# Kernel tuning notes

Hardware: AMD Instinct MI355X
Metric: run time of the kernel (lower is better)

The kernel has to match this reference:

```python
import jax, jax.numpy as jnp
import numpy as np

N = 50000   # num nodes
E = 400000  # num edges (avg degree 8)
D = 256     # in_channels
H = 256     # hidden_channels
C = 64      # out_channels
K = 2       # k_hops


def setup_inputs() -> dict:
    key = jax.random.key(0)
    ks = jax.random.split(key, 10)
    x = jax.random.normal(ks[0], (N, D), dtype=jnp.float32)
    edge_index = jax.random.randint(ks[1], (2, E), 0, N, dtype=jnp.int32)
    s = 0.05
    # per-hop linears of the single H2GCNConv (weights stored [in, out])
    W0 = jax.random.normal(ks[2], (D, H), jnp.float32) * s
    W1 = jax.random.normal(ks[3], (D, H), jnp.float32) * s
    W2 = jax.random.normal(ks[4], (D, H), jnp.float32) * s
    b0 = jnp.zeros((H,), jnp.float32)
    b1 = jnp.zeros((H,), jnp.float32)
    b2 = jnp.zeros((H,), jnp.float32)
    # classifier: h2_out_dim = H*(K+1) = 768 -> C
    Wc = jax.random.normal(ks[5], (H * (K + 1), C), jnp.float32) * s
    bc = jnp.zeros((C,), jnp.float32)
    return {"x": x, "edge_index": edge_index, "num_nodes": N,
            "W0": W0, "b0": b0, "W1": W1, "b1": b1, "W2": W2, "b2": b2,
            "Wc": Wc, "bc": bc}


def _normalize_adj(edge_index, num_nodes):
    # add self loops, then D^{-1/2} A D^{-1/2} edge weights
    loops = jnp.arange(num_nodes, dtype=edge_index.dtype)
    ei = jnp.concatenate([edge_index, jnp.stack([loops, loops])], axis=1)
    row, col = ei[0], ei[1]
    deg = jax.ops.segment_sum(jnp.ones(row.shape[0], jnp.float32), row,
                              num_segments=num_nodes)
    dis = jnp.where(deg > 0, deg ** -0.5, 0.0)  # inf -> 0 for isolated nodes
    return ei, dis[row] * dis[col]


def _sparse_mm(edge_index, edge_weight, x, num_nodes):
    # gather -> scale -> scatter-add (COO SpMM)
    row, col = edge_index[0], edge_index[1]
    msg = x[col] * edge_weight[:, None]  # [E', F]
    return jax.ops.segment_sum(msg, row, num_segments=num_nodes)


def reference(x, edge_index, num_nodes, W0, b0, W1, b1, W2, b2, Wc, bc):
    ei, ew = _normalize_adj(edge_index, num_nodes)
    # H2GCNConv: ego + k-hop aggregates, each through its own linear, concat
    outs = [x @ W0 + b0]
    cur = x
    for Wk, bk in ((W1, b1), (W2, b2)):
        cur = _sparse_mm(ei, ew, cur, num_nodes)
        outs.append(cur @ Wk + bk)
    h = jax.nn.relu(jnp.concatenate(outs, axis=1))  # [N, 3H]
    # dropout p=0 / eval mode -> identity
    return h @ Wc + bc
```

## Files before the change

kernel.cpp:

```cpp
#include <hip/hip_runtime.h>


#define FD 256
#define CO 64
#define SB 512

using frag_ab = __attribute__((ext_vector_type(8))) short;
using f32x4   = __attribute__((ext_vector_type(4))) float;
typedef unsigned short u16;
typedef unsigned int   u32;

__device__ __forceinline__ u16 f2bf(float f) {
    u32 u = __builtin_bit_cast(u32, f);
    return (u16)((u + 0x7FFFu + ((u >> 16) & 1u)) >> 16);
}
__device__ __forceinline__ float bfl(u32 packed) {
    return __builtin_bit_cast(float, packed << 16);
}
__device__ __forceinline__ float bfh(u32 packed) {
    return __builtin_bit_cast(float, packed & 0xFFFF0000u);
}

__device__ __forceinline__ void gll16(const void* g, void* l) {
    __builtin_amdgcn_global_load_lds(
        (const __attribute__((address_space(1))) u32*)g,
        (__attribute__((address_space(3))) u32*)l, 16, 0, 0);
}

#define BAR()  __builtin_amdgcn_s_barrier()
#define WLG0() asm volatile("s_waitcnt lgkmcnt(0)" ::: "memory")
#define WVM0() asm volatile("s_waitcnt vmcnt(0)" ::: "memory")
#define WVM2() asm volatile("s_waitcnt vmcnt(2)" ::: "memory")

__global__ void zerok(int4* __restrict__ deg4, int4* __restrict__ fill4, int n4) {
    int i = blockIdx.x * blockDim.x + threadIdx.x;
    int4 z = make_int4(0, 0, 0, 0);
    if (i < n4) { deg4[i] = z; fill4[i] = z; }
}
__global__ void count_kernel(const int* __restrict__ ei0, int* deg, int e) {
    int i = blockIdx.x * blockDim.x + threadIdx.x;
    if (i < e) atomicAdd(&deg[ei0[i]], 1);
}
__global__ void scan1(const int* __restrict__ deg, int* __restrict__ rowptr,
                      int* __restrict__ bsum, float* __restrict__ dis, int n) {
    __shared__ int sh[SB];
    int tid = threadIdx.x;
    int i = blockIdx.x * SB + tid;
    int v = (i < n) ? deg[i] + 1 : 0;
    if (i < n) dis[i] = rsqrtf((float)v);
    sh[tid] = v;
    __syncthreads();
    for (int off = 1; off < SB; off <<= 1) {
        int add = (tid >= off) ? sh[tid - off] : 0;
        __syncthreads();
        sh[tid] += add;
        __syncthreads();
    }
    if (i < n) rowptr[i] = sh[tid] - v;
    if (tid == SB - 1) bsum[blockIdx.x] = sh[tid];
}
__global__ void scan2(const int* __restrict__ bsum, int* __restrict__ bscan, int nb) {
    __shared__ int sh[128];
    int tid = threadIdx.x;
    int v = (tid < nb) ? bsum[tid] : 0;
    sh[tid] = v;
    __syncthreads();
    for (int off = 1; off < 128; off <<= 1) {
        int add = (tid >= off) ? sh[tid - off] : 0;
        __syncthreads();
        sh[tid] += add;
        __syncthreads();
    }
    if (tid < nb) bscan[tid] = sh[tid] - v;
    if (tid == nb - 1) bscan[nb] = sh[tid];
}
__global__ void scan3(int* rowptr, const int* __restrict__ bscan, int n, int nb) {
    int i = blockIdx.x * 256 + threadIdx.x;
    if (i < n) rowptr[i] += bscan[i / SB];
    if (i == n) rowptr[n] = bscan[nb];
}
__global__ void fill_kernel(const int* __restrict__ ei, const float* __restrict__ dis,
                            const int* __restrict__ rowptr, int* fill,
                            int2* __restrict__ cw, int e, int n) {
    int i = blockIdx.x * blockDim.x + threadIdx.x;
    if (i >= e + n) return;
    int r, c;
    if (i < e) { r = ei[i]; c = ei[e + i]; }
    else       { r = i - e; c = r; }
    float w = dis[r] * dis[c];
    int pos = rowptr[r] + atomicAdd(&fill[r], 1);
    int2 p; p.x = c; p.y = __float_as_int(w);
    cw[pos] = p;
}

__global__ void conv_kernel(const float* __restrict__ x, u16* __restrict__ xb, int total4) {
    int i = blockIdx.x * blockDim.x + threadIdx.x;
    if (i < total4) {
        float4 v = ((const float4*)x)[i];
        ushort4 o;
        o.x = f2bf(v.x); o.y = f2bf(v.y); o.z = f2bf(v.z); o.w = f2bf(v.w);
        ((ushort4*)xb)[i] = o;
    }
}
__global__ void wtrans_kernel(const float* __restrict__ W0, const float* __restrict__ W1,
                              const float* __restrict__ W2, const float* __restrict__ Wc,
                              u16* __restrict__ WkT, u16* __restrict__ WcT) {
    __shared__ u16 tl[64][65];
    int b = blockIdx.x;
    const float* src; u16* dst; int R, C, r0, c0;
    if (b < 48) {
        int k = b >> 4, t = b & 15;
        src = (k == 0) ? W0 : (k == 1) ? W1 : W2;
        dst = WkT + k * 65536;
        R = 256; C = 256; r0 = (t >> 2) * 64; c0 = (t & 3) * 64;
    } else {
        int t = b - 48;
        src = Wc; dst = WcT;
        R = 768; C = 64; r0 = t * 64; c0 = 0;
    }
    int tid = threadIdx.x;
    int rr = tid >> 4, cc = (tid & 15) * 4;
    #pragma unroll
    for (int it = 0; it < 4; ++it) {
        int r = it * 16 + rr;
        float4 v = *(const float4*)(src + (size_t)(r0 + r) * C + c0 + cc);
        tl[cc + 0][r] = f2bf(v.x); tl[cc + 1][r] = f2bf(v.y);
        tl[cc + 2][r] = f2bf(v.z); tl[cc + 3][r] = f2bf(v.w);
    }
    __syncthreads();
    #pragma unroll
    for (int it = 0; it < 4; ++it) {
        int crow = it * 16 + rr;
        ushort4 o;
        o.x = tl[crow][cc + 0]; o.y = tl[crow][cc + 1];
        o.z = tl[crow][cc + 2]; o.w = tl[crow][cc + 3];
        *(ushort4*)(dst + (size_t)(c0 + crow) * R + r0 + cc) = o;
    }
}

__global__ void spmm_bf16(const int* __restrict__ rowptr, const int2* __restrict__ cw,
                          const u16* __restrict__ xb, u16* __restrict__ outb, int n) {
    int tid = threadIdx.x;
    int lane = tid & 63;
    int row = blockIdx.x * 8 + ((tid >> 6) << 1) + (lane >> 5);
    if (row >= n) return;
    int l32 = lane & 31;
    int p0 = rowptr[row], p1 = rowptr[row + 1];
    float a[8];
    #pragma unroll
    for (int j = 0; j < 8; ++j) a[j] = 0.f;

    int p = p0;
    for (; p + 8 <= p1; p += 8) {
        int2 cwv[8]; uint4 v[8];
        #pragma unroll
        for (int u = 0; u < 8; ++u) cwv[u] = cw[p + u];
        #pragma unroll
        for (int u = 0; u < 8; ++u)
            v[u] = *(const uint4*)(xb + (size_t)cwv[u].x * FD + l32 * 8);
        #pragma unroll
        for (int u = 0; u < 8; ++u) {
            float wt = __int_as_float(cwv[u].y);
            a[0] += wt * bfl(v[u].x); a[1] += wt * bfh(v[u].x);
            a[2] += wt * bfl(v[u].y); a[3] += wt * bfh(v[u].y);
            a[4] += wt * bfl(v[u].z); a[5] += wt * bfh(v[u].z);
            a[6] += wt * bfl(v[u].w); a[7] += wt * bfh(v[u].w);
        }
    }
    for (; p + 2 <= p1; p += 2) {
        int2 cwv[2]; uint4 v[2];
        #pragma unroll
        for (int u = 0; u < 2; ++u) cwv[u] = cw[p + u];
        #pragma unroll
        for (int u = 0; u < 2; ++u)
            v[u] = *(const uint4*)(xb + (size_t)cwv[u].x * FD + l32 * 8);
        #pragma unroll
        for (int u = 0; u < 2; ++u) {
            float wt = __int_as_float(cwv[u].y);
            a[0] += wt * bfl(v[u].x); a[1] += wt * bfh(v[u].x);
            a[2] += wt * bfl(v[u].y); a[3] += wt * bfh(v[u].y);
            a[4] += wt * bfl(v[u].z); a[5] += wt * bfh(v[u].z);
            a[6] += wt * bfl(v[u].w); a[7] += wt * bfh(v[u].w);
        }
    }
    for (; p < p1; ++p) {
        int2 cwv = cw[p];
        float wt = __int_as_float(cwv.y);
        uint4 v = *(const uint4*)(xb + (size_t)cwv.x * FD + l32 * 8);
        a[0] += wt * bfl(v.x); a[1] += wt * bfh(v.x);
        a[2] += wt * bfl(v.y); a[3] += wt * bfh(v.y);
        a[4] += wt * bfl(v.z); a[5] += wt * bfh(v.z);
        a[6] += wt * bfl(v.w); a[7] += wt * bfh(v.w);
    }
    uint4 o;
    o.x = (u32)f2bf(a[0]) | ((u32)f2bf(a[1]) << 16);
    o.y = (u32)f2bf(a[2]) | ((u32)f2bf(a[3]) << 16);
    o.z = (u32)f2bf(a[4]) | ((u32)f2bf(a[5]) << 16);
    o.w = (u32)f2bf(a[6]) | ((u32)f2bf(a[7]) << 16);
    *(uint4*)(outb + (size_t)row * FD + l32 * 8) = o;
}

__launch_bounds__(256, 2)
__global__ void fused_gemm(const u16* __restrict__ xb, const u16* __restrict__ agg1b,
                           const u16* __restrict__ agg2b, const u16* __restrict__ WkT,
                           const float* __restrict__ b0, const float* __restrict__ b1,
                           const float* __restrict__ b2, const u16* __restrict__ WcT,
                           const float* __restrict__ bc, float* __restrict__ out, int n) {
    __shared__ __align__(16) char lds[73728];
    char* Tl = lds + 40960;

    const int tid = threadIdx.x;
    const int w = tid >> 6, l = tid & 63;
    const int l4 = l >> 4, lm = l & 15;
    const int row0 = blockIdx.x * 64;
    const int rr = w * 16 + lm;

    f32x4 oacc[4];
    #pragma unroll
    for (int am = 0; am < 4; ++am) oacc[am] = (f32x4)(0.f);

    for (int seg = 0; seg < 3; ++seg) {
        const u16* inb = (seg == 0) ? xb : (seg == 1) ? agg1b : agg2b;
        const u16* WT  = WkT + (size_t)seg * 65536;
        const float* bk = (seg == 0) ? b0 : (seg == 1) ? b1 : b2;

        auto stageB = [&](int kt, int pb) {
            {
                int L = tid * 16;
                int r = L >> 6, s = (L >> 4) & 3;
                int gr = row0 + r; if (gr > n - 1) gr = n - 1;
                gll16(inb + (size_t)gr * FD + kt * 32 + (s ^ (r & 3)) * 8,
                      lds + pb * 4096 + L);
            }
            #pragma unroll
            for (int i = 0; i < 4; ++i) {
                int L = tid * 16 + i * 4096;
                int j = L >> 6, s = (L >> 4) & 3;
                gll16(WT + (size_t)j * FD + kt * 32 + (s ^ (j & 3)) * 8,
                      lds + 8192 + pb * 16384 + L);
            }
        };

        f32x4 acc[4][4];
        #pragma unroll
        for (int jm = 0; jm < 4; ++jm)
            #pragma unroll
            for (int rn = 0; rn < 4; ++rn) acc[jm][rn] = (f32x4)(0.f);

        stageB(0, 0);
        WVM0();
        BAR();

        #pragma unroll
        for (int kt = 0; kt < 8; ++kt) {
            char* curA = lds + (kt & 1) * 4096;
            char* curW = lds + 8192 + (kt & 1) * 16384;
            if (kt < 7) stageB(kt + 1, (kt + 1) & 1);

            frag_ab af[4], bf_[4];
            #pragma unroll
            for (int jm = 0; jm < 4; ++jm) {
                int j = w * 64 + jm * 16 + lm;
                af[jm] = *(const frag_ab*)(curW + j * 64 + ((l4 ^ (j & 3)) << 4));
            }
            #pragma unroll
            for (int rn = 0; rn < 4; ++rn) {
                int r = rn * 16 + lm;
                bf_[rn] = *(const frag_ab*)(curA + r * 64 + ((l4 ^ (r & 3)) << 4));
            }
            #pragma unroll
            for (int jm = 0; jm < 4; ++jm)
                #pragma unroll
                for (int rn = 0; rn < 4; ++rn)
                    acc[jm][rn] = __builtin_amdgcn_mfma_f32_16x16x32_bf16(af[jm], bf_[rn], acc[jm][rn], 0, 0, 0);

            if (kt < 7) WVM0();
            WLG0();
            BAR();
        }

        auto stageC = [&](int kt2, int pb) {
            #pragma unroll
            for (int i = 0; i < 2; ++i) {
                int L = tid * 16 + i * 4096;
                int c = L >> 7, s = (L >> 4) & 7;
                gll16(WcT + (size_t)c * 768 + seg * 256 + kt2 * 64 + (s ^ (c & 7)) * 8,
                      lds + 8192 + pb * 8192 + L);
            }
        };
        stageC(0, 0);

        #pragma unroll
        for (int jm = 0; jm < 4; ++jm) {
            int j0 = w * 64 + jm * 16 + l4 * 4;
            float4 bb = *(const float4*)(bk + j0);
            #pragma unroll
            for (int rn = 0; rn < 4; ++rn) {
                int r = rn * 16 + lm;
                f32x4 v = acc[jm][rn];
                ushort4 p;
                p.x = f2bf(fmaxf(v[0] + bb.x, 0.f));
                p.y = f2bf(fmaxf(v[1] + bb.y, 0.f));
                p.z = f2bf(fmaxf(v[2] + bb.z, 0.f));
                p.w = f2bf(fmaxf(v[3] + bb.w, 0.f));
                *(ushort4*)(Tl + r * 512 + (((j0 >> 3) ^ (r & 7)) << 4) + (j0 & 7) * 2) = p;
            }
        }
        WLG0();
        BAR();

        #pragma unroll
        for (int kt2 = 0; kt2 < 4; ++kt2) {
            char* cw_ = lds + 8192 + (kt2 & 1) * 8192;
            if (kt2 < 3) {
                stageC(kt2 + 1, (kt2 + 1) & 1);
                WVM2();
            } else {
                WVM0();
            }
            BAR();
            #pragma unroll
            for (int kk2 = 0; kk2 < 2; ++kk2) {
                int g = kt2 * 8 + kk2 * 4 + l4;
                frag_ab bfr = *(const frag_ab*)(Tl + rr * 512 + ((g ^ (rr & 7)) << 4));
                #pragma unroll
                for (int am = 0; am < 4; ++am) {
                    int c = am * 16 + lm;
                    frag_ab afr = *(const frag_ab*)(cw_ + c * 128 + (((kk2 * 4 + l4) ^ (c & 7)) << 4));
                    oacc[am] = __builtin_amdgcn_mfma_f32_16x16x32_bf16(afr, bfr, oacc[am], 0, 0, 0);
                }
            }
            WLG0();
            BAR();
        }
    }

    int gr = row0 + rr;
    if (gr < n) {
        #pragma unroll
        for (int am = 0; am < 4; ++am) {
            float4 bb = *(const float4*)(bc + am * 16 + l4 * 4);
            float4 o;
            o.x = oacc[am][0] + bb.x;
            o.y = oacc[am][1] + bb.y;
            o.z = oacc[am][2] + bb.z;
            o.w = oacc[am][3] + bb.w;
            *(float4*)(out + (size_t)gr * CO + am * 16 + l4 * 4) = o;
        }
    }
}

extern "C" void kernel_launch(void* const* d_in, const int* in_sizes, int n_in,
                              void* d_out, int out_size, void* d_ws, size_t ws_size,
                              hipStream_t stream) {
    const float* x  = (const float*)d_in[0];
    const int*   ei = (const int*)d_in[1];
    const float* W0 = (const float*)d_in[3];
    const float* b0 = (const float*)d_in[4];
    const float* W1 = (const float*)d_in[5];
    const float* b1 = (const float*)d_in[6];
    const float* W2 = (const float*)d_in[7];
    const float* b2 = (const float*)d_in[8];
    const float* Wc = (const float*)d_in[9];
    const float* bc = (const float*)d_in[10];
    float* out = (float*)d_out;

    const int n  = in_sizes[0] / FD;
    const int e  = in_sizes[1] / 2;
    const int ep = e + n;
    const int nb = (n + SB - 1) / SB;

    char* ws = (char*)d_ws;
    size_t o = 0;
    auto take = [&](size_t nbytes) -> char* {
        char* p = ws + o;
        o += (nbytes + 255) & ~(size_t)255;
        return p;
    };
    int*   deg    = (int*)  take((size_t)n * 4);
    int*   fill   = (int*)  take((size_t)n * 4);
    float* dis    = (float*)take((size_t)n * 4);
    int*   rowptr = (int*)  take((size_t)(n + 1) * 4);
    int*   bsum   = (int*)  take((size_t)(nb + 1) * 4);
    int*   bscan  = (int*)  take((size_t)(nb + 1) * 4);
    int2*  cw     = (int2*) take((size_t)ep * 8);
    u16*   xb     = (u16*)  take((size_t)n * FD * 2);
    u16*   agg1b  = (u16*)  take((size_t)n * FD * 2);
    u16*   agg2b  = (u16*)  take((size_t)n * FD * 2);
    u16*   WkT    = (u16*)  take((size_t)3 * FD * FD * 2);
    u16*   WcT    = (u16*)  take((size_t)CO * 3 * FD * 2);
    (void)ws_size; (void)n_in; (void)out_size;

    const int n4 = (n + 3) / 4;
    zerok       <<<(n4 + 255) / 256, 256, 0, stream>>>((int4*)deg, (int4*)fill, n4);
    count_kernel<<<(e + 255) / 256, 256, 0, stream>>>(ei, deg, e);
    scan1       <<<nb, SB, 0, stream>>>(deg, rowptr, bsum, dis, n);
    scan2       <<<1, 128, 0, stream>>>(bsum, bscan, nb);
    scan3       <<<(n + 256) / 256, 256, 0, stream>>>(rowptr, bscan, n, nb);
    fill_kernel <<<(ep + 255) / 256, 256, 0, stream>>>(ei, dis, rowptr, fill, cw, e, n);

    const int total4 = n * FD / 4;
    conv_kernel  <<<(total4 + 255) / 256, 256, 0, stream>>>(x, xb, total4);
    wtrans_kernel<<<60, 256, 0, stream>>>(W0, W1, W2, Wc, WkT, WcT);

    spmm_bf16<<<(n + 7) / 8, 256, 0, stream>>>(rowptr, cw, xb, agg1b, n);
    spmm_bf16<<<(n + 7) / 8, 256, 0, stream>>>(rowptr, cw, agg1b, agg2b, n);

    fused_gemm<<<(n + 63) / 64, 256, 0, stream>>>(xb, agg1b, agg2b, WkT,
                                                  b0, b1, b2, WcT, bc, out, n);
}
```

Before: 197.3 us.

## Keep per-hop weights in registers and stage full A tiles in ping-pong LDS

The fused GEMM now holds each wave's slice of the per-hop weight matrix in registers, loading it directly from global memory and prefetching the next hop's weights during the epilogue. This replaces the double-buffered per-k-tile LDS staging of both weights and activations. The full 64x256 activation tile and the Wc slice are each staged once per segment into two 32KB halves of LDS that swap roles between segments. The aim is to cut barriers and LDS traffic per k-step, at the cost of heavy register pressure (32 fragments per thread) and less overlap between loads and compute.

Measured after the change: 246.2 us. +24.8%, slower.

```diff
diff --git a/kernel.cpp b/kernel.cpp
--- a/kernel.cpp
+++ b/kernel.cpp
@@ -30,7 +30,6 @@
 #define BAR()  __builtin_amdgcn_s_barrier()
 #define WLG0() asm volatile("s_waitcnt lgkmcnt(0)" ::: "memory")
 #define WVM0() asm volatile("s_waitcnt vmcnt(0)" ::: "memory")
-#define WVM2() asm volatile("s_waitcnt vmcnt(2)" ::: "memory")
 
 __global__ void zerok(int4* __restrict__ deg4, int4* __restrict__ fill4, int n4) {
     int i = blockIdx.x * blockDim.x + threadIdx.x;
@@ -206,89 +205,81 @@
                            const float* __restrict__ b0, const float* __restrict__ b1,
                            const float* __restrict__ b2, const u16* __restrict__ WcT,
                            const float* __restrict__ bc, float* __restrict__ out, int n) {
-    __shared__ __align__(16) char lds[73728];
-    char* Tl = lds + 40960;
-
+    __shared__ __align__(16) char lds[65536];
     const int tid = threadIdx.x;
     const int w = tid >> 6, l = tid & 63;
     const int l4 = l >> 4, lm = l & 15;
     const int row0 = blockIdx.x * 64;
     const int rr = w * 16 + lm;
 
+    auto stageA = [&](const u16* inb, char* dst) {
+        #pragma unroll
+        for (int i = 0; i < 8; ++i) {
+            int L = tid * 16 + i * 4096;
+            int r = L >> 9, g = (L >> 4) & 31;
+            int gr = row0 + r; if (gr > n - 1) gr = n - 1;
+            gll16(inb + (size_t)gr * FD + (g ^ (r & 7)) * 8, dst + L);
+        }
+    };
+    auto stageWc = [&](int seg, char* dst) {
+        #pragma unroll
+        for (int i = 0; i < 8; ++i) {
+            int L = tid * 16 + i * 4096;
+            int c = L >> 9, g = (L >> 4) & 31;
+            gll16(WcT + (size_t)c * 768 + seg * 256 + (g ^ (c & 7)) * 8, dst + L);
+        }
+    };
+
+    frag_ab wreg[4][8];
+    auto loadW = [&](int seg) {
+        const u16* WT = WkT + (size_t)seg * 65536;
+        #pragma unroll
+        for (int jm = 0; jm < 4; ++jm)
+            #pragma unroll
+            for (int kt = 0; kt < 8; ++kt)
+                wreg[jm][kt] = *(const frag_ab*)(WT + (size_t)(w * 64 + jm * 16 + lm) * FD + kt * 32 + l4 * 8);
+    };
+
     f32x4 oacc[4];
     #pragma unroll
     for (int am = 0; am < 4; ++am) oacc[am] = (f32x4)(0.f);
 
+    stageA(xb, lds);
+    loadW(0);
+    WVM0();
+    BAR();
+
+    #pragma unroll
     for (int seg = 0; seg < 3; ++seg) {
-        const u16* inb = (seg == 0) ? xb : (seg == 1) ? agg1b : agg2b;
-        const u16* WT  = WkT + (size_t)seg * 65536;
+        char* aR = lds + ((seg & 1) ? 32768 : 0);
+        char* tR = lds + ((seg & 1) ? 0 : 32768);
         const float* bk = (seg == 0) ? b0 : (seg == 1) ? b1 : b2;
 
-        auto stageB = [&](int kt, int pb) {
-            {
-                int L = tid * 16;
-                int r = L >> 6, s = (L >> 4) & 3;
-                int gr = row0 + r; if (gr > n - 1) gr = n - 1;
-                gll16(inb + (size_t)gr * FD + kt * 32 + (s ^ (r & 3)) * 8,
-                      lds + pb * 4096 + L);
-            }
-            #pragma unroll
-            for (int i = 0; i < 4; ++i) {
-                int L = tid * 16 + i * 4096;
-                int j = L >> 6, s = (L >> 4) & 3;
-                gll16(WT + (size_t)j * FD + kt * 32 + (s ^ (j & 3)) * 8,
-                      lds + 8192 + pb * 16384 + L);
-            }
-        };
-
         f32x4 acc[4][4];
         #pragma unroll
         for (int jm = 0; jm < 4; ++jm)
             #pragma unroll
             for (int rn = 0; rn < 4; ++rn) acc[jm][rn] = (f32x4)(0.f);
 
-        stageB(0, 0);
-        WVM0();
-        BAR();
-
         #pragma unroll
         for (int kt = 0; kt < 8; ++kt) {
-            char* curA = lds + (kt & 1) * 4096;
-            char* curW = lds + 8192 + (kt & 1) * 16384;
-            if (kt < 7) stageB(kt + 1, (kt + 1) & 1);
-
-            frag_ab af[4], bf_[4];
-            #pragma unroll
-            for (int jm = 0; jm < 4; ++jm) {
-                int j = w * 64 + jm * 16 + lm;
-                af[jm] = *(const frag_ab*)(curW + j * 64 + ((l4 ^ (j & 3)) << 4));
-            }
+            frag_ab bf_[4];
             #pragma unroll
             for (int rn = 0; rn < 4; ++rn) {
                 int r = rn * 16 + lm;
-                bf_[rn] = *(const frag_ab*)(curA + r * 64 + ((l4 ^ (r & 3)) << 4));
+                bf_[rn] = *(const frag_ab*)(aR + r * 512 + (((kt * 4 + l4) ^ (r & 7)) << 4));
             }
             #pragma unroll
             for (int jm = 0; jm < 4; ++jm)
                 #pragma unroll
                 for (int rn = 0; rn < 4; ++rn)
-                    acc[jm][rn] = __builtin_amdgcn_mfma_f32_16x16x32_bf16(af[jm], bf_[rn], acc[jm][rn], 0, 0, 0);
-
-            if (kt < 7) WVM0();
-            WLG0();
-            BAR();
-        }
-
-        auto stageC = [&](int kt2, int pb) {
-            #pragma unroll
-            for (int i = 0; i < 2; ++i) {
-                int L = tid * 16 + i * 4096;
-                int c = L >> 7, s = (L >> 4) & 7;
-                gll16(WcT + (size_t)c * 768 + seg * 256 + kt2 * 64 + (s ^ (c & 7)) * 8,
-                      lds + 8192 + pb * 8192 + L);
-            }
-        };
-        stageC(0, 0);
+                    acc[jm][rn] = __builtin_amdgcn_mfma_f32_16x16x32_bf16(wreg[jm][kt], bf_[rn], acc[jm][rn], 0, 0, 0);
+        }
+        WLG0();
+        BAR();
+
+        stageWc(seg, aR);
+        if (seg < 2) loadW(seg + 1);
 
         #pragma unroll
         for (int jm = 0; jm < 4; ++jm) {
@@ -303,34 +294,29 @@
                 p.y = f2bf(fmaxf(v[1] + bb.y, 0.f));
                 p.z = f2bf(fmaxf(v[2] + bb.z, 0.f));
                 p.w = f2bf(fmaxf(v[3] + bb.w, 0.f));
-                *(ushort4*)(Tl + r * 512 + (((j0 >> 3) ^ (r & 7)) << 4) + (j0 & 7) * 2) = p;
+                *(ushort4*)(tR + r * 512 + (((j0 >> 3) ^ (r & 7)) << 4) + (j0 & 7) * 2) = p;
             }
         }
+        WVM0();
         WLG0();
         BAR();
 
         #pragma unroll
-        for (int kt2 = 0; kt2 < 4; ++kt2) {
-            char* cw_ = lds + 8192 + (kt2 & 1) * 8192;
-            if (kt2 < 3) {
-                stageC(kt2 + 1, (kt2 + 1) & 1);
-                WVM2();
-            } else {
-                WVM0();
+        for (int ks = 0; ks < 8; ++ks) {
+            frag_ab tb = *(const frag_ab*)(tR + rr * 512 + (((ks * 4 + l4) ^ (rr & 7)) << 4));
+            #pragma unroll
+            for (int am = 0; am < 4; ++am) {
+                int c = am * 16 + lm;
+                frag_ab wc = *(const frag_ab*)(aR + c * 512 + (((ks * 4 + l4) ^ (c & 7)) << 4));
+                oacc[am] = __builtin_amdgcn_mfma_f32_16x16x32_bf16(wc, tb, oacc[am], 0, 0, 0);
             }
-            BAR();
-            #pragma unroll
-            for (int kk2 = 0; kk2 < 2; ++kk2) {
-                int g = kt2 * 8 + kk2 * 4 + l4;
-                frag_ab bfr = *(const frag_ab*)(Tl + rr * 512 + ((g ^ (rr & 7)) << 4));
-                #pragma unroll
-                for (int am = 0; am < 4; ++am) {
-                    int c = am * 16 + lm;
-                    frag_ab afr = *(const frag_ab*)(cw_ + c * 128 + (((kk2 * 4 + l4) ^ (c & 7)) << 4));
-                    oacc[am] = __builtin_amdgcn_mfma_f32_16x16x32_bf16(afr, bfr, oacc[am], 0, 0, 0);
-                }
-            }
-            WLG0();
+        }
+        WLG0();
+        BAR();
+
+        if (seg < 2) {
+            stageA((seg == 0) ? agg1b : agg2b, tR);
+            WVM0();
             BAR();
         }
     }
```

## Deepen fused GEMM prefetch pipeline and load full Wc slice per segment

Applied to the files above, without the earlier changes.

Reworks the fused GEMM's load schedule. The first two k-tiles of the next segment are now prefetched while the current segment finishes, so the wait at each k-step is vmcnt(5) rather than a full drain. The classifier-weight slice for each segment is loaded into LDS in one piece, replacing a double-buffered 4-step loop and removing the extra barriers. The LDS swizzle is changed from XOR to a rotate pattern on the Wc and T tiles and dropped entirely on the A and W tiles. That removal risks bank conflicts on those reads.

After: 203.2 us. 1.03x slower.

```diff
diff --git a/kernel.cpp b/kernel.cpp
--- a/kernel.cpp
+++ b/kernel.cpp
@@ -30,7 +30,7 @@
 #define BAR()  __builtin_amdgcn_s_barrier()
 #define WLG0() asm volatile("s_waitcnt lgkmcnt(0)" ::: "memory")
 #define WVM0() asm volatile("s_waitcnt vmcnt(0)" ::: "memory")
-#define WVM2() asm volatile("s_waitcnt vmcnt(2)" ::: "memory")
+#define WVM5() asm volatile("s_waitcnt vmcnt(5)" ::: "memory")
 
 __global__ void zerok(int4* __restrict__ deg4, int4* __restrict__ fill4, int n4) {
     int i = blockIdx.x * blockDim.x + threadIdx.x;
@@ -207,7 +207,9 @@
                            const float* __restrict__ b2, const u16* __restrict__ WcT,
                            const float* __restrict__ bc, float* __restrict__ out, int n) {
     __shared__ __align__(16) char lds[73728];
-    char* Tl = lds + 40960;
+    char* ppA = lds;
+    char* ppW = lds + 8192;
+    char* Tl  = lds + 40960;
 
     const int tid = threadIdx.x;
     const int w = tid >> 6, l = tid & 63;
@@ -215,58 +217,65 @@
     const int row0 = blockIdx.x * 64;
     const int rr = w * 16 + lm;
 
+    auto stageB = [&](const u16* inb, const u16* WT, int kt, int pb) {
+        {
+            int L = tid * 16;
+            int r = L >> 6, ch = (L >> 4) & 3;
+            int gr = row0 + r; if (gr > n - 1) gr = n - 1;
+            gll16(inb + (size_t)gr * FD + kt * 32 + ch * 8, ppA + pb * 4096 + L);
+        }
+        #pragma unroll
+        for (int i = 0; i < 4; ++i) {
+            int L = i * 4096 + tid * 16;
+            int j = L >> 6, ch = (L >> 4) & 3;
+            gll16(WT + (size_t)j * FD + kt * 32 + ch * 8, ppW + pb * 16384 + L);
+        }
+    };
+    auto stageWc = [&](int seg) {
+        #pragma unroll
+        for (int i = 0; i < 8; ++i) {
+            int L = i * 4096 + tid * 16;
+            int c = L >> 9, g = (L >> 4) & 31;
+            int kb = (g - 4 * (c & 7)) & 31;
+            gll16(WcT + (size_t)c * 768 + seg * 256 + kb * 8, ppW + L);
+        }
+    };
+
     f32x4 oacc[4];
     #pragma unroll
     for (int am = 0; am < 4; ++am) oacc[am] = (f32x4)(0.f);
+
+    stageB(xb, WkT, 0, 0);
+    stageB(xb, WkT, 1, 1);
 
     for (int seg = 0; seg < 3; ++seg) {
         const u16* inb = (seg == 0) ? xb : (seg == 1) ? agg1b : agg2b;
         const u16* WT  = WkT + (size_t)seg * 65536;
         const float* bk = (seg == 0) ? b0 : (seg == 1) ? b1 : b2;
 
-        auto stageB = [&](int kt, int pb) {
-            {
-                int L = tid * 16;
-                int r = L >> 6, s = (L >> 4) & 3;
-                int gr = row0 + r; if (gr > n - 1) gr = n - 1;
-                gll16(inb + (size_t)gr * FD + kt * 32 + (s ^ (r & 3)) * 8,
-                      lds + pb * 4096 + L);
-            }
-            #pragma unroll
-            for (int i = 0; i < 4; ++i) {
-                int L = tid * 16 + i * 4096;
-                int j = L >> 6, s = (L >> 4) & 3;
-                gll16(WT + (size_t)j * FD + kt * 32 + (s ^ (j & 3)) * 8,
-                      lds + 8192 + pb * 16384 + L);
-            }
-        };
-
         f32x4 acc[4][4];
         #pragma unroll
         for (int jm = 0; jm < 4; ++jm)
             #pragma unroll
             for (int rn = 0; rn < 4; ++rn) acc[jm][rn] = (f32x4)(0.f);
 
-        stageB(0, 0);
-        WVM0();
-        BAR();
-
         #pragma unroll
         for (int kt = 0; kt < 8; ++kt) {
-            char* curA = lds + (kt & 1) * 4096;
-            char* curW = lds + 8192 + (kt & 1) * 16384;
-            if (kt < 7) stageB(kt + 1, (kt + 1) & 1);
+            if (kt < 7) WVM5(); else WVM0();
+            BAR();
+            char* curA = ppA + (kt & 1) * 4096;
+            char* curW = ppW + (kt & 1) * 16384;
 
             frag_ab af[4], bf_[4];
             #pragma unroll
             for (int jm = 0; jm < 4; ++jm) {
                 int j = w * 64 + jm * 16 + lm;
-                af[jm] = *(const frag_ab*)(curW + j * 64 + ((l4 ^ (j & 3)) << 4));
+                af[jm] = *(const frag_ab*)(curW + j * 64 + l4 * 16);
             }
             #pragma unroll
             for (int rn = 0; rn < 4; ++rn) {
                 int r = rn * 16 + lm;
-                bf_[rn] = *(const frag_ab*)(curA + r * 64 + ((l4 ^ (r & 3)) << 4));
+                bf_[rn] = *(const frag_ab*)(curA + r * 64 + l4 * 16);
             }
             #pragma unroll
             for (int jm = 0; jm < 4; ++jm)
@@ -274,25 +283,17 @@
                 for (int rn = 0; rn < 4; ++rn)
                     acc[jm][rn] = __builtin_amdgcn_mfma_f32_16x16x32_bf16(af[jm], bf_[rn], acc[jm][rn], 0, 0, 0);
 
-            if (kt < 7) WVM0();
             WLG0();
             BAR();
-        }
-
-        auto stageC = [&](int kt2, int pb) {
-            #pragma unroll
-            for (int i = 0; i < 2; ++i) {
-                int L = tid * 16 + i * 4096;
-                int c = L >> 7, s = (L >> 4) & 7;
-                gll16(WcT + (size_t)c * 768 + seg * 256 + kt2 * 64 + (s ^ (c & 7)) * 8,
-                      lds + 8192 + pb * 8192 + L);
-            }
-        };
-        stageC(0, 0);
+            if (kt < 6) stageB(inb, WT, kt + 2, kt & 1);
+        }
+
+        stageWc(seg);
 
         #pragma unroll
         for (int jm = 0; jm < 4; ++jm) {
             int j0 = w * 64 + jm * 16 + l4 * 4;
+            int cb = j0 >> 3;
             float4 bb = *(const float4*)(bk + j0);
             #pragma unroll
             for (int rn = 0; rn < 4; ++rn) {
@@ -303,35 +304,34 @@
                 p.y = f2bf(fmaxf(v[1] + bb.y, 0.f));
                 p.z = f2bf(fmaxf(v[2] + bb.z, 0.f));
                 p.w = f2bf(fmaxf(v[3] + bb.w, 0.f));
-                *(ushort4*)(Tl + r * 512 + (((j0 >> 3) ^ (r & 7)) << 4) + (j0 & 7) * 2) = p;
+                int g = (cb + 4 * (r & 7)) & 31;
+                *(ushort4*)(Tl + r * 512 + g * 16 + (j0 & 7) * 2) = p;
             }
         }
+        WVM0();
         WLG0();
         BAR();
 
         #pragma unroll
-        for (int kt2 = 0; kt2 < 4; ++kt2) {
-            char* cw_ = lds + 8192 + (kt2 & 1) * 8192;
-            if (kt2 < 3) {
-                stageC(kt2 + 1, (kt2 + 1) & 1);
-                WVM2();
-            } else {
-                WVM0();
+        for (int ks = 0; ks < 8; ++ks) {
+            int gt = ((ks * 4 + l4) + 4 * (rr & 7)) & 31;
+            frag_ab tb = *(const frag_ab*)(Tl + rr * 512 + gt * 16);
+            #pragma unroll
+            for (int am = 0; am < 4; ++am) {
+                int c = am * 16 + lm;
+                int gw = ((ks * 4 + l4) + 4 * (c & 7)) & 31;
+                frag_ab wc = *(const frag_ab*)(ppW + c * 512 + gw * 16);
+                oacc[am] = __builtin_amdgcn_mfma_f32_16x16x32_bf16(wc, tb, oacc[am], 0, 0, 0);
             }
-            BAR();
-            #pragma unroll
-            for (int kk2 = 0; kk2 < 2; ++kk2) {
-                int g = kt2 * 8 + kk2 * 4 + l4;
-                frag_ab bfr = *(const frag_ab*)(Tl + rr * 512 + ((g ^ (rr & 7)) << 4));
-                #pragma unroll
-                for (int am = 0; am < 4; ++am) {
-                    int c = am * 16 + lm;
-                    frag_ab afr = *(const frag_ab*)(cw_ + c * 128 + (((kk2 * 4 + l4) ^ (c & 7)) << 4));
-                    oacc[am] = __builtin_amdgcn_mfma_f32_16x16x32_bf16(afr, bfr, oacc[am], 0, 0, 0);
-                }
-            }
-            WLG0();
-            BAR();
+        }
+        WLG0();
+        BAR();
+
+        if (seg < 2) {
+            const u16* inn = (seg == 0) ? agg1b : agg2b;
+            const u16* WTn = WkT + (size_t)(seg + 1) * 65536;
+            stageB(inn, WTn, 0, 0);
+            stageB(inn, WTn, 1, 1);
         }
     }
 
```
